# Optimization experiments

Measured on AMD Instinct MI355X. Metric: run time of the kernel, lower is better.

Reference implementation:

```python
import jax, jax.numpy as jnp
import numpy as np

DIM = 2048
HEADS = 32
DIM_HEAD = 64
FF_INNER = DIM * 4
SCALE_BASE = 512
FUSED = HEADS * DIM_HEAD + DIM_HEAD + DIM_HEAD + FF_INNER * 2  # 18560


def setup_inputs() -> dict:
    key = jax.random.key(0)
    k1, k2, k3, k4 = jax.random.split(key, 4)
    b, n = 2, 2048
    x = jax.random.normal(k1, (b, n, DIM), dtype=jnp.float32)
    W_fused = jax.random.normal(k2, (FUSED, DIM), dtype=jnp.float32) * 0.02
    W_attn_out = jax.random.normal(k3, (DIM, HEADS * DIM_HEAD), dtype=jnp.float32) * 0.02
    W_ff_out = jax.random.normal(k4, (DIM, FF_INNER), dtype=jnp.float32) * 0.02
    gamma = jnp.ones((DIM,), dtype=jnp.float32)
    return {"x": x, "gamma": gamma, "W_fused": W_fused,
            "W_attn_out": W_attn_out, "W_ff_out": W_ff_out}


def _rotate_half(t):
    t1, t2 = jnp.split(t, 2, axis=-1)
    return jnp.concatenate((-t2, t1), axis=-1)


def _rotary(n, dtype):
    # xpos rotary embeddings: freqs [n, dim_head], scale [n, dim_head]
    inv_freq = 1.0 / (10000.0 ** (jnp.arange(0, DIM_HEAD, 2, dtype=jnp.float32) / DIM_HEAD))
    t = jnp.arange(n, dtype=jnp.float32)
    freqs = t[:, None] * inv_freq[None, :]
    freqs = jnp.concatenate((freqs, freqs), axis=-1)
    power = (t - n // 2) / SCALE_BASE
    scale_base_vec = (jnp.arange(0, DIM_HEAD, 2, dtype=jnp.float32) + 0.4 * DIM_HEAD) / (1.4 * DIM_HEAD)
    scale = scale_base_vec[None, :] ** power[:, None]
    scale = jnp.concatenate((scale, scale), axis=-1)
    return freqs.astype(dtype), scale.astype(dtype)


def _apply_rotary(pos, t, scale):
    return t * jnp.cos(pos) * scale + _rotate_half(t) * jnp.sin(pos) * scale


def reference(x, gamma, W_fused, W_attn_out, W_ff_out):
    b, n, d = x.shape
    # LayerNorm (beta fixed at zero)
    mu = jnp.mean(x, axis=-1, keepdims=True)
    var = jnp.mean((x - mu) ** 2, axis=-1, keepdims=True)
    xn = (x - mu) * jax.lax.rsqrt(var + 1e-5) * gamma

    # fused QKV + FF projection
    proj = jnp.einsum('bnd,fd->bnf', xn, W_fused)
    attn_inner = HEADS * DIM_HEAD
    q = proj[..., :attn_inner]
    k = proj[..., attn_inner:attn_inner + DIM_HEAD]
    v = proj[..., attn_inner + DIM_HEAD:attn_inner + 2 * DIM_HEAD]
    ff = proj[..., attn_inner + 2 * DIM_HEAD:]

    # multi-query attention with xpos rotary
    q = q.reshape(b, n, HEADS, DIM_HEAD).transpose(0, 2, 1, 3)  # b h n d
    q = q * (DIM_HEAD ** -0.5)
    pos, scale = _rotary(n, x.dtype)
    q = _apply_rotary(pos, q, scale)          # broadcasts over b,h
    k = _apply_rotary(pos, k, 1.0 / scale)    # k is [b, n, dim_head]

    sim = jnp.einsum('bhid,bjd->bhij', q, k)
    causal_mask = jnp.triu(jnp.ones((n, n), dtype=bool), k=1)
    sim = jnp.where(causal_mask, -jnp.finfo(sim.dtype).max, sim)
    attn = jax.nn.softmax(sim, axis=-1)
    out = jnp.einsum('bhij,bjd->bhid', attn, v)
    out = out.transpose(0, 2, 1, 3).reshape(b, n, attn_inner)
    attn_out = jnp.einsum('bnf,df->bnd', out, W_attn_out)

    # SwiGLU FF
    ff_x, gate = jnp.split(ff, 2, axis=-1)
    ff_hidden = jax.nn.silu(gate) * ff_x
    ff_out = jnp.einsum('bnf,df->bnd', ff_hidden, W_ff_out)

    return attn_out + ff_out
```

## Files before the change

### kernel.cpp

```cpp
#include <hip/hip_runtime.h>
#include <cstdint>
#include <cstddef>

typedef __bf16 bf16;
typedef float f32x4 __attribute__((ext_vector_type(4)));
typedef bf16  bf16x4 __attribute__((ext_vector_type(4)));
typedef bf16  bf16x8 __attribute__((ext_vector_type(8)));

#define DIMD   2048
#define HEADS  32
#define DH     64
#define FFI    8192
#define FUSEDN 18560
#define FUSEDP 18688
#define BB     2
#define NN     2048
#define MROWS  4096
#define K2     10240

__device__ __forceinline__ void gl_lds16(const void* g, void* l) {
  __builtin_amdgcn_global_load_lds(
      (__attribute__((address_space(1))) void*)const_cast<void*>(g),
      (__attribute__((address_space(3))) void*)l, 16, 0, 0);
}

template <int THREADS>
__device__ __forceinline__ void stage_i(const bf16* g, long ldk,
                                        bf16* region, int instr, int tid) {
  int row = instr * (THREADS / 8) + (tid >> 3);
  int cs  = (tid & 7) ^ (row & 7);
  gl_lds16(g + (size_t)row * ldk + cs * 8,
           region + (size_t)instr * (THREADS * 8) + (size_t)(tid & ~63) * 8);
}

struct SrcT { const bf16* g; long ldk; };

template <typename FA, typename FB>
__device__ __forceinline__ void gemm_2ph(FA fa, FB fb, const int NT,
    bf16* As, bf16* Bs, f32x4 (&acc)[4][4],
    const int tid, const int wrow, const int nbase, const int l15, const int h4)
{
  const char* aP[2]; const char* bP[2];
  const int arow = wrow + l15, brow = nbase + l15;
#pragma unroll
  for (int ks = 0; ks < 2; ks++) {
    aP[ks] = (const char*)As + arow * 128 + (((ks * 4 + h4) ^ (arow & 7)) * 16);
    bP[ks] = (const char*)Bs + brow * 128 + (((ks * 4 + h4) ^ (brow & 7)) * 16);
  }
  for (int t = 0; t < NT; ++t) {
    __syncthreads();
    {
      auto a = fa(t); auto b = fb(t);
#pragma unroll
      for (int q = 0; q < 4; q++) stage_i<256>(a.g, a.ldk, As, q, tid);
#pragma unroll
      for (int q = 0; q < 4; q++) stage_i<256>(b.g, b.ldk, Bs, q, tid);
    }
    __syncthreads();
#pragma unroll
    for (int ks = 0; ks < 2; ks++) {
      bf16x8 af[4], bfr[4];
#pragma unroll
      for (int m_ = 0; m_ < 4; m_++) af[m_]  = *(const bf16x8*)(aP[ks] + m_ * 2048);
#pragma unroll
      for (int n_ = 0; n_ < 4; n_++) bfr[n_] = *(const bf16x8*)(bP[ks] + n_ * 2048);
#pragma unroll
      for (int m_ = 0; m_ < 4; m_++)
#pragma unroll
        for (int n_ = 0; n_ < 4; n_++)
          acc[m_][n_] = __builtin_amdgcn_mfma_f32_16x16x32_bf16(af[m_], bfr[n_], acc[m_][n_], 0, 0, 0);
    }
  }
}

__global__ __launch_bounds__(256) void k_prep(const float* __restrict__ x,
                                              const float* __restrict__ g,
                                              bf16* __restrict__ xn,
                                              const float* __restrict__ Wf,
                                              bf16* __restrict__ wfb) {
  __shared__ float rs[8];
  const int bid = blockIdx.x, t = threadIdx.x;
  if (bid < MROWS) {
    int row = bid;
    const float4* xr = (const float4*)(x + (size_t)row * DIMD);
    float4 a = xr[t*2], b = xr[t*2+1];
    float s  = a.x+a.y+a.z+a.w + b.x+b.y+b.z+b.w;
    float s2 = a.x*a.x+a.y*a.y+a.z*a.z+a.w*a.w + b.x*b.x+b.y*b.y+b.z*b.z+b.w*b.w;
    for (int o = 1; o < 64; o <<= 1) { s += __shfl_xor(s, o); s2 += __shfl_xor(s2, o); }
    if ((t & 63) == 0) { rs[t>>6] = s; rs[4 + (t>>6)] = s2; }
    __syncthreads();
    s = rs[0]+rs[1]+rs[2]+rs[3]; s2 = rs[4]+rs[5]+rs[6]+rs[7];
    float mu = s * (1.f/DIMD);
    float var = s2 * (1.f/DIMD) - mu*mu;
    float rstd = rsqrtf(var + 1e-5f);
    const float4* gr = (const float4*)g;
    float4 g0 = gr[t*2], g1 = gr[t*2+1];
    bf16x8 o;
    o[0]=(bf16)((a.x-mu)*rstd*g0.x); o[1]=(bf16)((a.y-mu)*rstd*g0.y);
    o[2]=(bf16)((a.z-mu)*rstd*g0.z); o[3]=(bf16)((a.w-mu)*rstd*g0.w);
    o[4]=(bf16)((b.x-mu)*rstd*g1.x); o[5]=(bf16)((b.y-mu)*rstd*g1.y);
    o[6]=(bf16)((b.z-mu)*rstd*g1.z); o[7]=(bf16)((b.w-mu)*rstd*g1.w);
    *(bf16x8*)(xn + (size_t)row * DIMD + t*8) = o;
  } else {
    const long total8 = (long)FUSEDN * DIMD / 8;
    const long stride = 2048L * 256;
    for (long i = (long)(bid - MROWS) * 256 + t; i < total8; i += stride) {
      long e = i << 3;
      int p = (int)(e >> 11);
      int c = (int)(e & 2047);
      int orig;
      if (p < 2176) orig = p;
      else {
        int q = p - 2176, gg = q >> 6, o2 = q & 63;
        orig = (o2 < 32) ? (2176 + gg * 32 + o2) : (2176 + 8192 + gg * 32 + (o2 - 32));
      }
      const float* src = Wf + (size_t)orig * 2048 + c;
      float4 v0 = *(const float4*)src;
      float4 v1 = *(const float4*)(src + 4);
      bf16x8 o8;
      o8[0]=(bf16)v0.x; o8[1]=(bf16)v0.y; o8[2]=(bf16)v0.z; o8[3]=(bf16)v0.w;
      o8[4]=(bf16)v1.x; o8[5]=(bf16)v1.y; o8[6]=(bf16)v1.z; o8[7]=(bf16)v1.w;
      *(bf16x8*)(wfb + e) = o8;
    }
  }
}

__global__ __launch_bounds__(256, 3) void k_gemm1(const bf16* __restrict__ xn,
                                                  const bf16* __restrict__ wf,
                                                  bf16* __restrict__ q_raw,
                                                  bf16* __restrict__ k_buf,
                                                  bf16* __restrict__ v_t,
                                                  bf16* __restrict__ ffh) {
  __shared__ bf16 As[128*64];
  __shared__ bf16 Bs[128*64];
  const int tid = threadIdx.x, w = tid >> 6, l = tid & 63;
  const int l15 = l & 15, h4 = l >> 4;
  const int wrow = (w >> 1) * 64, nbase = (w & 1) * 64;
  const int bid = blockIdx.x;
  const int bs = (bid & 7) * 584 + (bid >> 3);
  const int mt = bs & 31, nt = bs >> 5;
  const int m0 = mt * 128, f0 = nt * 128;

  f32x4 acc[4][4];
#pragma unroll
  for (int i = 0; i < 4; i++)
#pragma unroll
    for (int j = 0; j < 4; j++) acc[i][j] = (f32x4){0.f,0.f,0.f,0.f};

  auto fa = [&](int t) -> SrcT { return SrcT{ xn + (size_t)m0 * DIMD + t * 64, (long)DIMD }; };
  auto fb = [&](int t) -> SrcT { return SrcT{ wf + (size_t)f0 * DIMD + t * 64, (long)DIMD }; };
  gemm_2ph(fa, fb, DIMD / 64, As, Bs, acc, tid, wrow, nbase, l15, h4);

  if (nt < 16) {
    const int hh = (f0 + nbase) >> 6;
    float invf[2], lsb[2];
#pragma unroll
    for (int nf = 0; nf < 2; nf++) {
      int i = nf*16 + l15;
      invf[nf] = exp2f((float)i * -0.4152410118f);
      lsb[nf]  = __log2f(((float)(2*i) + 25.6f) * (1.f/89.6f));
    }
#pragma unroll
    for (int m_ = 0; m_ < 4; m_++)
#pragma unroll
      for (int j = 0; j < 4; j++) {
        int m = m0 + wrow + m_*16 + h4*4 + j;
        int n = m & 2047, b = m >> 11;
        float power = ((float)n - 1024.f) * (1.f/512.f);
        bf16* qrow = q_raw + (((size_t)(b*HEADS + hh) * NN + n) << 6);
#pragma unroll
        for (int nf = 0; nf < 2; nf++) {
          float t1 = acc[m_][nf][j], t2 = acc[m_][nf+2][j];
          float sn, cs; __sincosf((float)n * invf[nf], &sn, &cs);
          float sc = exp2f(power * lsb[nf]) * 0.125f;
          int i = nf*16 + l15;
          qrow[i]      = (bf16)((t1*cs - t2*sn) * sc);
          qrow[i + 32] = (bf16)((t2*cs + t1*sn) * sc);
        }
      }
  } else if (nt == 16) {
    if (nbase == 0) {
      float invf[2], lsb[2];
#pragma unroll
      for (int nf = 0; nf < 2; nf++) {
        int i = nf*16 + l15;
        invf[nf] = exp2f((float)i * -0.4152410118f);
        lsb[nf]  = __log2f(((float)(2*i) + 25.6f) * (1.f/89.6f));
      }
#pragma unroll
      for (int m_ = 0; m_ < 4; m_++)
#pragma unroll
        for (int j = 0; j < 4; j++) {
          int m = m0 + wrow + m_*16 + h4*4 + j;
          int n = m & 2047, b = m >> 11;
          float power = ((float)n - 1024.f) * (1.f/512.f);
          bf16* krow = k_buf + (((size_t)(b*NN + n)) << 6);
#pragma unroll
          for (int nf = 0; nf < 2; nf++) {
            float t1 = acc[m_][nf][j], t2 = acc[m_][nf+2][j];
            float sn, cs; __sincosf((float)n * invf[nf], &sn, &cs);
            float sc = exp2f(-power * lsb[nf]);
            int i = nf*16 + l15;
            krow[i]      = (bf16)((t1*cs - t2*sn) * sc);
            krow[i + 32] = (bf16)((t2*cs + t1*sn) * sc);
          }
        }
    } else {
#pragma unroll
      for (int m_ = 0; m_ < 4; m_++)
#pragma unroll
        for (int nf = 0; nf < 4; nf++) {
          int d = nf*16 + l15;
#pragma unroll
          for (int j = 0; j < 4; j++) {
            int m = m0 + wrow + m_*16 + h4*4 + j;
            int n = m & 2047, b = m >> 11;
            v_t[(((size_t)(b*DH + d)) << 11) + n] = (bf16)acc[m_][nf][j];
          }
        }
    }
  } else {
    int base = f0 + nbase;
    if (base < FUSEDN) {
      int g = (base - 2176) >> 6;
#pragma unroll
      for (int m_ = 0; m_ < 4; m_++)
#pragma unroll
        for (int nf = 0; nf < 2; nf++) {
          int xc = g*32 + nf*16 + l15;
#pragma unroll
          for (int j = 0; j < 4; j++) {
            int m = m0 + wrow + m_*16 + h4*4 + j;
            float xv = acc[m_][nf][j];
            float gv = acc[m_][nf+2][j];
            float sv = gv * (1.f / (1.f + __expf(-gv)));
            ffh[((size_t)m << 13) + xc] = (bf16)(sv * xv);
          }
        }
    }
  }
}

__global__ __launch_bounds__(256, 3) void k_gemm2(const bf16* __restrict__ u_o,
                                                  const bf16* __restrict__ ffh,
                                                  const bf16* __restrict__ wcat,
                                                  float* __restrict__ out,
                                                  float* __restrict__ part) {
  __shared__ bf16 As[128*64];
  __shared__ bf16 Bs[128*64];
  const int tid = threadIdx.x, w = tid >> 6, l = tid & 63;
  const int l15 = l & 15, h4 = l >> 4;
  const int wrow = (w >> 1) * 64, nbase = (w & 1) * 64;
  const int bid = blockIdx.x;
  const int kk = bid >> 9;
  const int inner = bid & 511;
  const int bs = (inner & 7) * 64 + (inner >> 3);
  const int mt = bs & 31, nt = bs >> 5;
  const int m0 = mt * 128, f0 = nt * 128;
  const int T0 = kk * 80;

  f32x4 acc[4][4];
#pragma unroll
  for (int i = 0; i < 4; i++)
#pragma unroll
    for (int j = 0; j < 4; j++) acc[i][j] = (f32x4){0.f,0.f,0.f,0.f};

  auto fa = [&](int t) -> SrcT {
    int tt = t + T0;
    if (tt < 32) return SrcT{ u_o + (size_t)m0 * DIMD + tt * 64, (long)DIMD };
    return SrcT{ ffh + (size_t)m0 * FFI + (tt - 32) * 64, (long)FFI };
  };
  auto fb = [&](int t) -> SrcT { return SrcT{ wcat + (size_t)f0 * K2 + (t + T0) * 64, (long)K2 }; };
  gemm_2ph(fa, fb, 80, As, Bs, acc, tid, wrow, nbase, l15, h4);

  float* dst = kk ? part : out;
#pragma unroll
  for (int m_ = 0; m_ < 4; m_++)
#pragma unroll
    for (int nf = 0; nf < 4; nf++) {
      int fcol = f0 + nbase + nf*16 + l15;
#pragma unroll
      for (int j = 0; j < 4; j++) {
        int m = m0 + wrow + m_*16 + h4*4 + j;
        dst[(size_t)m * DIMD + fcol] = acc[m_][nf][j];
      }
    }
}

__global__ void k_addout(float* __restrict__ out, const float* __restrict__ part, long total4) {
  long stride = (long)gridDim.x * blockDim.x;
  for (long i = (long)blockIdx.x * blockDim.x + threadIdx.x; i < total4; i += stride) {
    long e = i << 2;
    float4 a = *(const float4*)(out + e);
    float4 b = *(const float4*)(part + e);
    float4 r; r.x = a.x + b.x; r.y = a.y + b.y; r.z = a.z + b.z; r.w = a.w + b.w;
    *(float4*)(out + e) = r;
  }
}

__global__ __launch_bounds__(256) void k_attn_cvt(const bf16* __restrict__ qbuf,
                                                  const bf16* __restrict__ kbuf,
                                                  const bf16* __restrict__ vtb,
                                                  bf16* __restrict__ uo,
                                                  const float* __restrict__ Wao,
                                                  const float* __restrict__ Wff,
                                                  bf16* __restrict__ wcat) {
  __shared__ bf16 Qs[128*64];
  __shared__ bf16 Ks[64*64];
  __shared__ bf16 Vs[64*64];
  const int tid = threadIdx.x, w = tid >> 6, l = tid & 63;
  const int l15 = l & 15, h4 = l >> 4;
  const int bid = blockIdx.x;

  if (bid >= 1024) {
    const long stride = 1024L * 256;
    long i0 = (long)(bid - 1024) * 256 + tid;
    for (long i = i0; i < (long)DIMD * DIMD / 8; i += stride) {
      long e = i << 3;
      long r = e >> 11; int c = (int)(e & 2047);
      float4 v0 = *(const float4*)(Wao + e);
      float4 v1 = *(const float4*)(Wao + e + 4);
      bf16x8 o;
      o[0]=(bf16)v0.x; o[1]=(bf16)v0.y; o[2]=(bf16)v0.z; o[3]=(bf16)v0.w;
      o[4]=(bf16)v1.x; o[5]=(bf16)v1.y; o[6]=(bf16)v1.z; o[7]=(bf16)v1.w;
      *(bf16x8*)(wcat + r * (long)K2 + c) = o;
    }
    for (long i = i0; i < (long)DIMD * FFI / 8; i += stride) {
      long e = i << 3;
      long r = e >> 13; int c = (int)(e & 8191);
      float4 v0 = *(const float4*)(Wff + e);
      float4 v1 = *(const float4*)(Wff + e + 4);
      bf16x8 o;
      o[0]=(bf16)v0.x; o[1]=(bf16)v0.y; o[2]=(bf16)v0.z; o[3]=(bf16)v0.w;
      o[4]=(bf16)v1.x; o[5]=(bf16)v1.y; o[6]=(bf16)v1.z; o[7]=(bf16)v1.w;
      *(bf16x8*)(wcat + r * (long)K2 + DIMD + c) = o;
    }
    return;
  }

  const int qt = 15 - (bid & 15);
  const int bh = bid >> 4;
  const int h = bh & (HEADS - 1), b = bh >> 5;
  const int q0 = qt * 128;
  const bf16* Qg = qbuf + ((size_t)(b*HEADS + h) * NN + q0) * DH;
  const bf16* Kg = kbuf + (size_t)b * NN * DH;
  const bf16* Vg = vtb + (size_t)b * DH * NN;

#pragma unroll
  for (int c = 0; c < 4; c++) {
    int chunk = c*256 + tid;
    int r = chunk >> 3, cc = chunk & 7;
    int col8 = (cc ^ (r & 7)) << 3;
    gl_lds16(Qg + (size_t)r*DH + col8, Qs + ((size_t)(chunk & ~63) << 3));
  }
  __syncthreads();

  const int wq0 = q0 + w*32;
  bf16x8 qfr[2][2];
#pragma unroll
  for (int qf = 0; qf < 2; qf++)
#pragma unroll
    for (int c = 0; c < 2; c++) {
      int row = w*32 + qf*16 + l15;
      int x = (64*c + 16*h4) ^ (16*(row & 7));
      qfr[qf][c] = *(const bf16x8*)((const char*)Qs + row*128 + x);
    }

  f32x4 zf = {0.f,0.f,0.f,0.f};
  f32x4 o_[2][4];
#pragma unroll
  for (int qf = 0; qf < 2; qf++)
#pragma unroll
    for (int nf = 0; nf < 4; nf++) o_[qf][nf] = zf;
  float mrun[2] = {-3e38f, -3e38f};
  float lrun[2] = {0.f, 0.f};

  const int nsteps = (q0 + 128) >> 6;
  for (int kt = 0; kt < nsteps; kt++) {
    const int kv0 = kt << 6;
    stage_i<256>(Kg + (size_t)kv0 * DH, DH, Ks, 0, tid);
    stage_i<256>(Kg + (size_t)kv0 * DH, DH, Ks, 1, tid);
    stage_i<256>(Vg + kv0, NN, Vs, 0, tid);
    stage_i<256>(Vg + kv0, NN, Vs, 1, tid);
    __syncthreads();
    if (kv0 <= wq0 + 31) {
      bf16x8 ka[4][2];
#pragma unroll
      for (int kvf = 0; kvf < 4; kvf++)
#pragma unroll
        for (int c = 0; c < 2; c++) {
          int r = kvf*16 + l15;
          int x = (64*c + 16*h4) ^ (16*(r & 7));
          ka[kvf][c] = *(const bf16x8*)((const char*)Ks + r*128 + x);
        }
      f32x4 st[4][2];
#pragma unroll
      for (int kvf = 0; kvf < 4; kvf++)
#pragma unroll
        for (int qf = 0; qf < 2; qf++) {
          f32x4 s = __builtin_amdgcn_mfma_f32_16x16x32_bf16(ka[kvf][0], qfr[qf][0], zf, 0, 0, 0);
          s = __builtin_amdgcn_mfma_f32_16x16x32_bf16(ka[kvf][1], qfr[qf][1], s, 0, 0, 0);
          st[kvf][qf] = s;
        }
      if (kv0 + 63 > wq0) {
#pragma unroll
        for (int kvf = 0; kvf < 4; kvf++)
#pragma unroll
          for (int j = 0; j < 4; j++) {
            int kvg = kv0 + kvf*16 + h4*4 + j;
#pragma unroll
            for (int qf = 0; qf < 2; qf++) {
              int qg = wq0 + qf*16 + l15;
              if (kvg > qg) st[kvf][qf][j] = -3e38f;
            }
          }
      }
      bf16x8 pa[2][2];
#pragma unroll
      for (int qf = 0; qf < 2; qf++) {
        float vmax = -3e38f;
#pragma unroll
        for (int kvf = 0; kvf < 4; kvf++)
#pragma unroll
          for (int j = 0; j < 4; j++) vmax = fmaxf(vmax, st[kvf][qf][j]);
        vmax = fmaxf(vmax, __shfl_xor(vmax, 16));
        vmax = fmaxf(vmax, __shfl_xor(vmax, 32));
        float mnew = fmaxf(mrun[qf], vmax);
        float corr = __expf(mrun[qf] - mnew);
        float ps = 0.f;
        float pv_[16];
#pragma unroll
        for (int kvf = 0; kvf < 4; kvf++)
#pragma unroll
          for (int j = 0; j < 4; j++) {
            float p = __expf(st[kvf][qf][j] - mnew);
            pv_[kvf*4 + j] = p; ps += p;
          }
        ps += __shfl_xor(ps, 16);
        ps += __shfl_xor(ps, 32);
        lrun[qf] = lrun[qf]*corr + ps;
        mrun[qf] = mnew;
        bf16x8 t0, t1;
#pragma unroll
        for (int i = 0; i < 8; i++) { t0[i] = (bf16)pv_[i]; t1[i] = (bf16)pv_[8+i]; }
        pa[qf][0] = t0; pa[qf][1] = t1;
#pragma unroll
        for (int j = 0; j < 4; j++) {
          float cj = __shfl(corr, (l & 48) | (h4*4 + j), 64);
#pragma unroll
          for (int nf = 0; nf < 4; nf++) o_[qf][nf][j] *= cj;
        }
      }
#pragma unroll
      for (int nf = 0; nf < 4; nf++) {
        int d_ = nf*16 + l15;
        int swz = 16*(d_ & 7);
        const char* vrow = (const char*)Vs + d_*128;
#pragma unroll
        for (int hc = 0; hc < 2; hc++) {
          bf16x4 v0 = *(const bf16x4*)(vrow + ((hc*64 + 8*h4) ^ swz));
          bf16x4 v1 = *(const bf16x4*)(vrow + ((hc*64 + 32 + 8*h4) ^ swz));
          bf16x8 vb = __builtin_shufflevector(v0, v1, 0,1,2,3,4,5,6,7);
#pragma unroll
          for (int qf = 0; qf < 2; qf++)
            o_[qf][nf] = __builtin_amdgcn_mfma_f32_16x16x32_bf16(pa[qf][hc], vb, o_[qf][nf], 0, 0, 0);
        }
      }
    }
    __syncthreads();
  }
#pragma unroll
  for (int qf = 0; qf < 2; qf++) {
    float inv = 1.f / lrun[qf];
#pragma unroll
    for (int j = 0; j < 4; j++) {
      float ij = __shfl(inv, (l & 48) | (h4*4 + j), 64);
      int qg = wq0 + qf*16 + h4*4 + j;
      size_t rowoff = (size_t)(b*NN + qg) * DIMD + h*DH;
#pragma unroll
      for (int nf = 0; nf < 4; nf++)
        uo[rowoff + nf*16 + l15] = (bf16)(o_[qf][nf][j] * ij);
    }
  }
}

extern "C" void kernel_launch(void* const* d_in, const int* in_sizes, int n_in,
                              void* d_out, int out_size, void* d_ws, size_t ws_size,
                              hipStream_t stream) {
  const float* x     = (const float*)d_in[0];
  const float* gamma = (const float*)d_in[1];
  const float* Wf    = (const float*)d_in[2];
  const float* Wao   = (const float*)d_in[3];
  const float* Wff   = (const float*)d_in[4];
  float* out = (float*)d_out;
  char* ws = (char*)d_ws;

  size_t o = 0;
  bf16* wfb     = (bf16*)(ws + o); o += (size_t)FUSEDP * DIMD * 2;
  bf16* wcat    = wfb;
  bf16* xn      = (bf16*)(ws + o); o += (size_t)MROWS * DIMD * 2;
  bf16* q_raw   = (bf16*)(ws + o); o += (size_t)BB*HEADS*NN*DH * 2;
  bf16* k_buf   = (bf16*)(ws + o); o += (size_t)BB*NN*DH * 2;
  bf16* v_t     = (bf16*)(ws + o); o += (size_t)BB*DH*NN * 2;
  bf16* ffh     = (bf16*)(ws + o); o += (size_t)MROWS * FFI * 2;
  bf16* u_o     = (bf16*)(ws + o); o += (size_t)MROWS * DIMD * 2;
  float* part   = (float*)xn;

  k_prep<<<MROWS + 2048, 256, 0, stream>>>(x, gamma, xn, Wf, wfb);
  k_gemm1<<<(FUSEDP/128)*(MROWS/128), 256, 0, stream>>>(xn, wfb, q_raw, k_buf, v_t, ffh);
  k_attn_cvt<<<2048, 256, 0, stream>>>(q_raw, k_buf, v_t, u_o, Wao, Wff, wcat);
  k_gemm2<<<2*(MROWS/128)*(DIMD/128), 256, 0, stream>>>(u_o, ffh, wcat, out, part);
  k_addout<<<2048, 256, 0, stream>>>(out, part, (long)MROWS*DIMD/4);
}
```

Measured before the change: 724.6 us.

## Double-buffer K/V tiles in attention loop with async prefetch

Attention K/V staging becomes a double buffer inside one shared array that reuses the Q region. The next tile's global-to-LDS loads are issued before computing on the current tile, with manual vmcnt waits and raw s_barrier replacing __syncthreads. This is meant to hide global load latency behind MFMA and softmax work. The risk is correctness: raw barriers and partial vmcnt waits depend on how many loads stage_i issues and on LDS visibility ordering.

```diff
diff --git a/kernel.cpp b/kernel.cpp
--- a/kernel.cpp
+++ b/kernel.cpp
@@ -305,9 +305,7 @@
                                                   const float* __restrict__ Wao,
                                                   const float* __restrict__ Wff,
                                                   bf16* __restrict__ wcat) {
-  __shared__ bf16 Qs[128*64];
-  __shared__ bf16 Ks[64*64];
-  __shared__ bf16 Vs[64*64];
+  __shared__ bf16 smem[16384];
   const int tid = threadIdx.x, w = tid >> 6, l = tid & 63;
   const int l15 = l & 15, h4 = l >> 4;
   const int bid = blockIdx.x;
@@ -351,7 +349,7 @@
     int chunk = c*256 + tid;
     int r = chunk >> 3, cc = chunk & 7;
     int col8 = (cc ^ (r & 7)) << 3;
-    gl_lds16(Qg + (size_t)r*DH + col8, Qs + ((size_t)(chunk & ~63) << 3));
+    gl_lds16(Qg + (size_t)r*DH + col8, smem + ((size_t)(chunk & ~63) << 3));
   }
   __syncthreads();
 
@@ -363,8 +361,12 @@
     for (int c = 0; c < 2; c++) {
       int row = w*32 + qf*16 + l15;
       int x = (64*c + 16*h4) ^ (16*(row & 7));
-      qfr[qf][c] = *(const bf16x8*)((const char*)Qs + row*128 + x);
-    }
+      qfr[qf][c] = *(const bf16x8*)((const char*)smem + row*128 + x);
+    }
+  __syncthreads();
+
+  bf16 *curK = smem,        *nxtK = smem + 4096;
+  bf16 *curV = smem + 8192, *nxtV = smem + 12288;
 
   f32x4 zf = {0.f,0.f,0.f,0.f};
   f32x4 o_[2][4];
@@ -376,13 +378,24 @@
   float lrun[2] = {0.f, 0.f};
 
   const int nsteps = (q0 + 128) >> 6;
+  stage_i<256>(Kg, DH, curK, 0, tid);
+  stage_i<256>(Kg, DH, curK, 1, tid);
+  stage_i<256>(Vg, NN, curV, 0, tid);
+  stage_i<256>(Vg, NN, curV, 1, tid);
+
   for (int kt = 0; kt < nsteps; kt++) {
     const int kv0 = kt << 6;
-    stage_i<256>(Kg + (size_t)kv0 * DH, DH, Ks, 0, tid);
-    stage_i<256>(Kg + (size_t)kv0 * DH, DH, Ks, 1, tid);
-    stage_i<256>(Vg + kv0, NN, Vs, 0, tid);
-    stage_i<256>(Vg + kv0, NN, Vs, 1, tid);
-    __syncthreads();
+    if (kt + 1 < nsteps) {
+      const int kv1 = kv0 + 64;
+      stage_i<256>(Kg + (size_t)kv1 * DH, DH, nxtK, 0, tid);
+      stage_i<256>(Kg + (size_t)kv1 * DH, DH, nxtK, 1, tid);
+      stage_i<256>(Vg + kv1, NN, nxtV, 0, tid);
+      stage_i<256>(Vg + kv1, NN, nxtV, 1, tid);
+      asm volatile("s_waitcnt vmcnt(4)" ::: "memory");
+    } else {
+      asm volatile("s_waitcnt vmcnt(0)" ::: "memory");
+    }
+    __builtin_amdgcn_s_barrier();
     if (kv0 <= wq0 + 31) {
       bf16x8 ka[4][2];
 #pragma unroll
@@ -391,7 +404,7 @@
         for (int c = 0; c < 2; c++) {
           int r = kvf*16 + l15;
           int x = (64*c + 16*h4) ^ (16*(r & 7));
-          ka[kvf][c] = *(const bf16x8*)((const char*)Ks + r*128 + x);
+          ka[kvf][c] = *(const bf16x8*)((const char*)curK + r*128 + x);
         }
       f32x4 st[4][2];
 #pragma unroll
@@ -455,7 +468,7 @@
       for (int nf = 0; nf < 4; nf++) {
         int d_ = nf*16 + l15;
         int swz = 16*(d_ & 7);
-        const char* vrow = (const char*)Vs + d_*128;
+        const char* vrow = (const char*)curV + d_*128;
 #pragma unroll
         for (int hc = 0; hc < 2; hc++) {
           bf16x4 v0 = *(const bf16x4*)(vrow + ((hc*64 + 8*h4) ^ swz));
@@ -467,7 +480,9 @@
         }
       }
     }
-    __syncthreads();
+    __builtin_amdgcn_s_barrier();
+    { bf16* t_ = curK; curK = nxtK; nxtK = t_; }
+    { bf16* t_ = curV; curV = nxtV; nxtV = t_; }
   }
 #pragma unroll
   for (int qf = 0; qf < 2; qf++) {
```

New measurement: 727.5 us. About the same (+0.4%).
